# Kernel tuning notes

Measured on AMD Instinct MI355X. Metric: run time of the kernel, lower is better.

## Reference

```python
import jax, jax.numpy as jnp
import numpy as np

N_HEAD = 16
HEAD_SIZE = 64  # n_embd // n_head = 1024 // 16


def setup_inputs() -> dict:
    key = jax.random.key(0)
    k1, k2 = jax.random.split(key)
    B, T, C = 2, 2048, 1024
    x = jax.random.normal(k1, (B, T, C), dtype=jnp.float32)
    w_attn = jax.random.normal(k2, (C, 3 * C), dtype=jnp.float32) * (C ** -0.5)
    b_attn = jnp.zeros((3 * C,), dtype=jnp.float32)
    return {"x": x, "w_attn": w_attn, "b_attn": b_attn}


def reference(x, w_attn, b_attn):
    B, T, C = x.shape
    qkv = x @ w_attn + b_attn  # [B, T, 3C]
    q, k, v = jnp.split(qkv, 3, axis=-1)
    # [B, T, H, D] -> [B, H, T, D]
    def heads(t):
        return t.reshape(B, T, N_HEAD, HEAD_SIZE).transpose(0, 2, 1, 3)
    q, k, v = heads(q), heads(k), heads(v)
    scale = HEAD_SIZE ** -0.5
    wei = jnp.einsum('bhqd,bhkd->bhqk', q, k) * scale  # [B, H, T, T]
    causal = jnp.tril(jnp.ones((T, T), dtype=bool))
    wei = jnp.where(causal, wei, -jnp.inf)
    wei = jax.nn.softmax(wei, axis=-1)
    out = jnp.einsum('bhqk,bhkd->bhqd', wei, v)  # [B, H, T, D]
    out = out.transpose(0, 2, 1, 3).reshape(B, T, C)
    return out
```

## Files before the change

kernel.cpp:

```cpp
#include <hip/hip_runtime.h>
#include <hip/hip_bf16.h>

#define BSZ 2
#define SEQ 2048
#define CDIM 1024
#define NHEAD 16
#define HDIM 64
#define M_GEMM (BSZ * SEQ)
#define N_GEMM (3 * CDIM)
#define K_GEMM CDIM
#define QK_PITCH (2 * CDIM)

typedef __attribute__((ext_vector_type(8))) short short8;
typedef __attribute__((ext_vector_type(4))) short short4v;
typedef __attribute__((ext_vector_type(4))) float f32x4;

__device__ __forceinline__ short bf16_rn(float f) {
    unsigned u = __builtin_bit_cast(unsigned, f);
    u += 0x7FFF + ((u >> 16) & 1);
    return (short)(u >> 16);
}

__device__ __forceinline__ void gl2lds16(const short* g, short* l) {
    __builtin_amdgcn_global_load_lds(
        (const __attribute__((address_space(1))) unsigned int*)g,
        (__attribute__((address_space(3))) unsigned int*)l, 16, 0, 0);
}

#define WAITV2() asm volatile("s_waitcnt vmcnt(2)")
#define WAITV3() asm volatile("s_waitcnt vmcnt(3)")
#define WAITV0() asm volatile("s_waitcnt vmcnt(0)")
#define LGKM0()  asm volatile("s_waitcnt lgkmcnt(0)")
#define SCB()    __builtin_amdgcn_sched_barrier(0)
#define BARRIER() __builtin_amdgcn_s_barrier()

__global__ __launch_bounds__(256) void cvt_fused(const float* __restrict__ X,
                                                 const float* __restrict__ W,
                                                 short* __restrict__ Xb,
                                                 short* __restrict__ WT) {
    const int tid = threadIdx.x;
    if (blockIdx.x < 2048) {
        size_t idx = ((size_t)blockIdx.x * 256 + tid) * 8;
        float4 a = *(const float4*)&X[idx];
        float4 b = *(const float4*)&X[idx + 4];
        short8 o;
        o[0] = bf16_rn(a.x); o[1] = bf16_rn(a.y); o[2] = bf16_rn(a.z); o[3] = bf16_rn(a.w);
        o[4] = bf16_rn(b.x); o[5] = bf16_rn(b.y); o[6] = bf16_rn(b.z); o[7] = bf16_rn(b.w);
        *(short8*)&Xb[idx] = o;
        return;
    }
    __shared__ short T[64][72];
    const int bid = blockIdx.x - 2048;
    const int n0 = (bid % 48) * 64;
    const int k0 = (bid / 48) * 64;
#pragma unroll
    for (int pass = 0; pass < 4; ++pass) {
        int i = pass * 256 + tid;
        int kr = i >> 4;
        int n4 = i & 15;
        float4 v = *(const float4*)&W[(size_t)(k0 + kr) * N_GEMM + n0 + n4 * 4];
        T[n4 * 4 + 0][kr] = bf16_rn(v.x);
        T[n4 * 4 + 1][kr] = bf16_rn(v.y);
        T[n4 * 4 + 2][kr] = bf16_rn(v.z);
        T[n4 * 4 + 3][kr] = bf16_rn(v.w);
    }
    __syncthreads();
#pragma unroll
    for (int pass = 0; pass < 2; ++pass) {
        int o = pass * 256 + tid;
        int nr = o >> 3;
        int c8 = o & 7;
        *(short8*)&WT[(size_t)(n0 + nr) * K_GEMM + k0 + c8 * 8] =
            *(const short8*)&T[nr][c8 * 8];
    }
}

__global__ __launch_bounds__(512, 2) void qkv_gemm_8ph(const short* __restrict__ A,
                                                       const short* __restrict__ Bt,
                                                       const float* __restrict__ bias,
                                                       short* __restrict__ Yqk,
                                                       short* __restrict__ Yv) {
    __shared__ short Asl[32768];
    __shared__ short Bsl[24576];

    const int tid  = threadIdx.x;
    const int w    = tid >> 6;
    const int lane = tid & 63;
    const int l16  = lane & 15;
    const int quad = lane >> 4;
    const int wm   = w >> 2;
    const int wn   = w & 3;
    const int ls   = lane >> 3;
    const int lc   = lane & 7;
    const int fsw  = l16 & 7;

    const int orig = blockIdx.y * 16 + blockIdx.x;
    const int xcd  = orig & 7;
    const int idx  = orig >> 3;
    const int bM   = ((xcd & 1) << 3) + (idx & 7);
    const int bN   = (xcd >> 1) * 4 + (idx >> 3);
    const int m0   = bM << 8;
    const int n0   = bN * 192;

    const short* Ab = A  + (size_t)m0 * K_GEMM;
    const short* Bb = Bt + (size_t)n0 * K_GEMM;

    f32x4 acc[8][3];
#pragma unroll
    for (int i = 0; i < 8; ++i)
#pragma unroll
        for (int j = 0; j < 3; ++j) acc[i][j] = (f32x4){0.f, 0.f, 0.f, 0.f};

    auto stageA = [&](int unit, int tt, int sbuf) {
#pragma unroll
        for (int i = 0; i < 2; ++i) {
            const int u0 = (i * 8 + w) * 8;
            const int tr = (u0 & 63) + ((u0 >> 6) << 7) + unit * 64;
            gl2lds16(Ab + (size_t)(tr + ls) * K_GEMM + tt * 64 + ((lc ^ ls) << 3),
                     &Asl[sbuf * 16384 + tr * 64]);
        }
    };
    auto stageBE = [&](int tt, int sbuf) {
#pragma unroll
        for (int i = 0; i < 2; ++i) {
            const int jb = i * 64 + w * 8;
            const int gr = (jb >> 5) * 48 + (jb & 31);
            gl2lds16(Bb + (size_t)(gr + ls) * K_GEMM + tt * 64 + ((lc ^ ls) << 3),
                     &Bsl[sbuf * 12288 + jb * 64]);
        }
    };
    auto stageBO = [&](int tt, int sbuf) {
        const int t8 = w * 8;
        const int jb = 128 + t8;
        const int gr = (t8 >> 4) * 48 + 32 + (t8 & 15);
        gl2lds16(Bb + (size_t)(gr + ls) * K_GEMM + tt * 64 + ((lc ^ ls) << 3),
                 &Bsl[sbuf * 12288 + jb * 64]);
    };
    auto rdA = [&](int ab, int mi, int ks) -> short8 {
        const int r = wm * 128 + mi * 16 + l16;
        return *(const short8*)&Asl[ab + r * 64 + ((ks * 4 + quad) ^ fsw) * 8];
    };
    auto rdB = [&](int bb, int ni, int ks) -> short8 {
        const int j = (ni < 2) ? (wn * 32 + ni * 16 + l16)
                               : (128 + wn * 16 + l16);
        return *(const short8*)&Bsl[bb + j * 64 + ((ks * 4 + quad) ^ fsw) * 8];
    };

    stageA(0, 0, 0);
    stageBE(0, 0);
    stageA(1, 0, 0);
    stageBO(0, 0);
    WAITV3();
    SCB(); BARRIER(); SCB();

    for (int t = 0; t < 16; ++t) {
        const int buf = t & 1;
        const int sb  = buf ^ 1;
        const int tn  = (t + 1) & 15;
        const int ab  = buf * 16384;
        const int bb  = buf * 12288;

        short8 Af[4][2], Bf[3][2];

#pragma unroll
        for (int mi = 0; mi < 4; ++mi)
#pragma unroll
            for (int ks = 0; ks < 2; ++ks) Af[mi][ks] = rdA(ab, mi, ks);
#pragma unroll
        for (int ni = 0; ni < 2; ++ni)
#pragma unroll
            for (int ks = 0; ks < 2; ++ks) Bf[ni][ks] = rdB(bb, ni, ks);
        stageA(0, tn, sb);
        SCB(); BARRIER(); LGKM0(); SCB();
        __builtin_amdgcn_s_setprio(1);
#pragma unroll
        for (int mi = 0; mi < 4; ++mi)
#pragma unroll
            for (int ni = 0; ni < 2; ++ni)
#pragma unroll
                for (int ks = 0; ks < 2; ++ks)
                    acc[mi][ni] = __builtin_amdgcn_mfma_f32_16x16x32_bf16(
                        Af[mi][ks], Bf[ni][ks], acc[mi][ni], 0, 0, 0);
        __builtin_amdgcn_s_setprio(0);
        WAITV2();
        SCB(); BARRIER(); SCB();

#pragma unroll
        for (int ks = 0; ks < 2; ++ks) Bf[2][ks] = rdB(bb, 2, ks);
        stageBE(tn, sb);
        SCB(); BARRIER(); LGKM0(); SCB();
        __builtin_amdgcn_s_setprio(1);
#pragma unroll
        for (int mi = 0; mi < 4; ++mi)
#pragma unroll
            for (int ks = 0; ks < 2; ++ks)
                acc[mi][2] = __builtin_amdgcn_mfma_f32_16x16x32_bf16(
                    Af[mi][ks], Bf[2][ks], acc[mi][2], 0, 0, 0);
        __builtin_amdgcn_s_setprio(0);
        SCB(); BARRIER(); SCB();

#pragma unroll
        for (int mi = 0; mi < 4; ++mi)
#pragma unroll
            for (int ks = 0; ks < 2; ++ks) Af[mi][ks] = rdA(ab, 4 + mi, ks);
        stageA(1, tn, sb);
        SCB(); BARRIER(); LGKM0(); SCB();
        __builtin_amdgcn_s_setprio(1);
#pragma unroll
        for (int mi = 0; mi < 4; ++mi)
#pragma unroll
            for (int ni = 0; ni < 2; ++ni)
#pragma unroll
                for (int ks = 0; ks < 2; ++ks)
                    acc[4 + mi][ni] = __builtin_amdgcn_mfma_f32_16x16x32_bf16(
                        Af[mi][ks], Bf[ni][ks], acc[4 + mi][ni], 0, 0, 0);
        __builtin_amdgcn_s_setprio(0);
        SCB(); BARRIER(); SCB();

        stageBO(tn, sb);
        SCB(); BARRIER(); SCB();
        __builtin_amdgcn_s_setprio(1);
#pragma unroll
        for (int mi = 0; mi < 4; ++mi)
#pragma unroll
            for (int ks = 0; ks < 2; ++ks)
                acc[4 + mi][2] = __builtin_amdgcn_mfma_f32_16x16x32_bf16(
                    Af[mi][ks], Bf[2][ks], acc[4 + mi][2], 0, 0, 0);
        __builtin_amdgcn_s_setprio(0);
        WAITV3();
        SCB(); BARRIER(); SCB();
    }
    WAITV0();

    const float log2e8 = 0.125f * 1.44269504f;
#pragma unroll
    for (int mi = 0; mi < 8; ++mi) {
#pragma unroll
        for (int ni = 0; ni < 3; ++ni) {
            const int colg = n0 + wn * 48 + ni * 16 + l16;
            const float bb2 = bias[colg];
            if (colg >= 2 * CDIM) {
                const int row0 = m0 + wm * 128 + mi * 16 + quad * 4;
                short4v pk;
#pragma unroll
                for (int r = 0; r < 4; ++r) pk[r] = bf16_rn(acc[mi][ni][r] + bb2);
                *(short4v*)&Yv[(size_t)(colg - 2 * CDIM) * M_GEMM + row0] = pk;
            } else {
                const float qs = (colg < CDIM) ? log2e8 : 1.0f;
#pragma unroll
                for (int r = 0; r < 4; ++r) {
                    const int row = m0 + wm * 128 + mi * 16 + quad * 4 + r;
                    Yqk[(size_t)row * QK_PITCH + colg] =
                        bf16_rn((acc[mi][ni][r] + bb2) * qs);
                }
            }
        }
    }
}

__global__ __launch_bounds__(256) void attn_mfma(const short* __restrict__ qk,
                                                 const short* __restrict__ vT,
                                                 float* __restrict__ out) {
    const int b = blockIdx.z;
    const int h = blockIdx.y;
    const int bx = blockIdx.x;
    const int u = h + 16 * b;
    const int band = u >> 3;
    const int base = (band & 2) ? ((bx + 16) & 31) : bx;
    const int qt = (band & 1) ? (31 - base) : base;
    const int tid = threadIdx.x;
    const int w = tid >> 6;
    const int lane = tid & 63;
    const int quad = lane >> 4;
    const int l16 = lane & 15;
    const int q0 = qt * 64;

    __shared__ short Ks[2][64 * 64];
    __shared__ short Vt[2][64 * 64];

    int koff[2], voff[2], ldso[2];
#pragma unroll
    for (int p = 0; p < 2; ++p) {
        int cid = p * 256 + w * 64 + lane;
        int row = cid >> 3;
        int hK = (row & 3) | (((row >> 3) & 1) << 2);
        int cK = (cid & 7) ^ hK;
        int cV = (cid & 7) ^ (row & 7);
        koff[p] = row * QK_PITCH + cK * 8;
        voff[p] = row * M_GEMM + cV * 8;
        ldso[p] = (p * 256 + w * 64) * 8;
    }

    const short* qrow = qk + (size_t)(b * SEQ + q0 + w * 16 + l16) * QK_PITCH + h * HDIM;
    short8 aq[2];
    aq[0] = *(const short8*)(qrow + quad * 8);
    aq[1] = *(const short8*)(qrow + 32 + quad * 8);

    float l_run = 0.f;
    f32x4 o_acc[4];
#pragma unroll
    for (int dt = 0; dt < 4; ++dt) o_acc[dt] = (f32x4){0.f, 0.f, 0.f, 0.f};

    const int qglob = q0 + w * 16 + l16;
    const short* kb0 = qk + (size_t)(b * SEQ) * QK_PITCH + CDIM + h * HDIM;
    const short* vb0 = vT + (size_t)(h * HDIM) * M_GEMM + b * SEQ;

    const int ksl = l16 & 7;

    const int Fq = ((l16 >> 2) << 3) + (l16 & 3);

#pragma unroll
    for (int p = 0; p < 2; ++p) {
        gl2lds16(kb0 + koff[p], &Ks[0][ldso[p]]);
        gl2lds16(vb0 + voff[p], &Vt[0][ldso[p]]);
    }
    __syncthreads();

    for (int kt = 0; kt <= qt; ++kt) {
        const int cur = kt & 1;

        if (kt < qt) {
            const short* kbase = kb0 + (size_t)(kt + 1) * 64 * QK_PITCH;
            const short* vbase = vb0 + (kt + 1) * 64;
#pragma unroll
            for (int p = 0; p < 2; ++p) {
                gl2lds16(kbase + koff[p], &Ks[cur ^ 1][ldso[p]]);
                gl2lds16(vbase + voff[p], &Vt[cur ^ 1][ldso[p]]);
            }
        }

        const short* KsC = Ks[cur];
        const short* VtC = Vt[cur];

        f32x4 s[4];
#pragma unroll
        for (int nt = 0; nt < 4; ++nt) s[nt] = (f32x4){0.f, 0.f, 0.f, 0.f};
        __builtin_amdgcn_s_setprio(1);
#pragma unroll
        for (int nt = 0; nt < 4; ++nt) {
            const int F  = (nt >> 1) * 32 + (nt & 1) * 4 + Fq;
            const int hF = (F & 3) | (((F >> 3) & 1) << 2);
#pragma unroll
            for (int ks = 0; ks < 2; ++ks) {
                short8 kf = *(const short8*)&KsC[F * 64 + (((ks * 4 + quad) ^ hF) * 8)];
                s[nt] = __builtin_amdgcn_mfma_f32_16x16x32_bf16(kf, aq[ks], s[nt], 0, 0, 0);
            }
        }
        __builtin_amdgcn_s_setprio(0);

        short8 pa0, pa1;
        float lsum = 0.f;
        if (kt < qt) {
#pragma unroll
            for (int nt = 0; nt < 4; ++nt)
#pragma unroll
                for (int r = 0; r < 4; ++r) {
                    float pp = __builtin_amdgcn_exp2f(s[nt][r]);
                    lsum += pp;
                    short pb = bf16_rn(pp);
                    if (nt < 2) pa0[(nt & 1) * 4 + r] = pb;
                    else        pa1[(nt & 1) * 4 + r] = pb;
                }
        } else {
#pragma unroll
            for (int nt = 0; nt < 4; ++nt)
#pragma unroll
                for (int r = 0; r < 4; ++r) {
                    int key = kt * 64 + (nt >> 1) * 32 + quad * 8 + (nt & 1) * 4 + r;
                    float pp = __builtin_amdgcn_exp2f(s[nt][r]);
                    pp = (key > qglob) ? 0.f : pp;
                    lsum += pp;
                    short pb = bf16_rn(pp);
                    if (nt < 2) pa0[(nt & 1) * 4 + r] = pb;
                    else        pa1[(nt & 1) * 4 + r] = pb;
                }
        }
        l_run += lsum;

        __builtin_amdgcn_s_setprio(1);
#pragma unroll
        for (int dt = 0; dt < 4; ++dt)
#pragma unroll
            for (int ks = 0; ks < 2; ++ks) {
                short8 bv = *(const short8*)&VtC[(dt * 16 + l16) * 64 +
                                                 ((ks * 4 + quad) ^ ksl) * 8];
                o_acc[dt] = __builtin_amdgcn_mfma_f32_16x16x32_bf16(
                    ks ? pa1 : pa0, bv, o_acc[dt], 0, 0, 0);
            }
        __builtin_amdgcn_s_setprio(0);

        __syncthreads();
    }

    float l = l_run;
    l += __shfl_xor(l, 16);
    l += __shfl_xor(l, 32);
#pragma unroll
    for (int r = 0; r < 4; ++r) {
        float lq = __shfl(l, quad * 4 + r);
        float inv = 1.f / lq;
        int row = q0 + w * 16 + quad * 4 + r;
        float* optr = out + (size_t)(b * SEQ + row) * CDIM + h * HDIM;
#pragma unroll
        for (int dt = 0; dt < 4; ++dt)
            optr[dt * 16 + l16] = o_acc[dt][r] * inv;
    }
}

extern "C" void kernel_launch(void* const* d_in, const int* in_sizes, int n_in,
                              void* d_out, int out_size, void* d_ws, size_t ws_size,
                              hipStream_t stream) {
    const float* x      = (const float*)d_in[0];
    const float* w_attn = (const float*)d_in[1];
    const float* b_attn = (const float*)d_in[2];
    float* out = (float*)d_out;

    short* qk  = (short*)d_ws;
    short* vT  = (short*)((char*)d_ws + 16777216);
    short* xb  = (short*)((char*)d_ws + 25165824);
    short* wT  = (short*)((char*)d_ws + 33554432);

    cvt_fused<<<2048 + 768, 256, 0, stream>>>(x, w_attn, xb, wT);

    dim3 g1(N_GEMM / 192, M_GEMM / 256);
    qkv_gemm_8ph<<<g1, 512, 0, stream>>>(xb, wT, b_attn, qk, vT);

    dim3 g2(SEQ / 64, NHEAD, BSZ);
    attn_mfma<<<g2, 256, 0, stream>>>(qk, vT, out);
}
```

Measured before the change: 152.5 us.

## Pair complementary causal query tiles in one 512-thread block sharing K/V loads

Each attention block now runs 8 waves covering two query tiles, bx and 31-bx, so causal work per block is balanced. The two tiles share the same double-buffered K/V LDS stages, which halves the global-to-LDS traffic per query tile. The grid is halved to 16x16x2, and the old band-based tile remapping is removed. In exchange, the waves on the short tile sit idle at barriers during the later iterations, and there are fewer, larger blocks to schedule.

```diff
diff --git a/kernel.cpp b/kernel.cpp
--- a/kernel.cpp
+++ b/kernel.cpp
@@ -258,40 +258,38 @@
     }
 }
 
-__global__ __launch_bounds__(256) void attn_mfma(const short* __restrict__ qk,
+__global__ __launch_bounds__(512) void attn_mfma(const short* __restrict__ qk,
                                                  const short* __restrict__ vT,
                                                  float* __restrict__ out) {
     const int b = blockIdx.z;
     const int h = blockIdx.y;
     const int bx = blockIdx.x;
-    const int u = h + 16 * b;
-    const int band = u >> 3;
-    const int base = (band & 2) ? ((bx + 16) & 31) : bx;
-    const int qt = (band & 1) ? (31 - base) : base;
     const int tid = threadIdx.x;
     const int w = tid >> 6;
+    const int ws = w >> 2;
+    const int wq = w & 3;
     const int lane = tid & 63;
     const int quad = lane >> 4;
     const int l16 = lane & 15;
-    const int q0 = qt * 64;
+
+    const int qts   = ws ? (31 - bx) : bx;
+    const int ktmax = 31 - bx;
+    const int q0 = qts * 64;
 
     __shared__ short Ks[2][64 * 64];
     __shared__ short Vt[2][64 * 64];
 
-    int koff[2], voff[2], ldso[2];
-#pragma unroll
-    for (int p = 0; p < 2; ++p) {
-        int cid = p * 256 + w * 64 + lane;
-        int row = cid >> 3;
-        int hK = (row & 3) | (((row >> 3) & 1) << 2);
-        int cK = (cid & 7) ^ hK;
-        int cV = (cid & 7) ^ (row & 7);
-        koff[p] = row * QK_PITCH + cK * 8;
-        voff[p] = row * M_GEMM + cV * 8;
-        ldso[p] = (p * 256 + w * 64) * 8;
-    }
-
-    const short* qrow = qk + (size_t)(b * SEQ + q0 + w * 16 + l16) * QK_PITCH + h * HDIM;
+    int koff, voff, ldso;
+    {
+        const int cid = tid;
+        const int row = cid >> 3;
+        const int hK = (row & 3) | (((row >> 3) & 1) << 2);
+        koff = row * QK_PITCH + (((cid & 7) ^ hK)) * 8;
+        voff = row * M_GEMM + (((cid & 7) ^ (row & 7))) * 8;
+        ldso = (w * 64) * 8;
+    }
+
+    const short* qrow = qk + (size_t)(b * SEQ + q0 + wq * 16 + l16) * QK_PITCH + h * HDIM;
     short8 aq[2];
     aq[0] = *(const short8*)(qrow + quad * 8);
     aq[1] = *(const short8*)(qrow + 32 + quad * 8);
@@ -301,7 +299,7 @@
 #pragma unroll
     for (int dt = 0; dt < 4; ++dt) o_acc[dt] = (f32x4){0.f, 0.f, 0.f, 0.f};
 
-    const int qglob = q0 + w * 16 + l16;
+    const int qglob = q0 + wq * 16 + l16;
     const short* kb0 = qk + (size_t)(b * SEQ) * QK_PITCH + CDIM + h * HDIM;
     const short* vb0 = vT + (size_t)(h * HDIM) * M_GEMM + b * SEQ;
 
@@ -309,85 +307,81 @@
 
     const int Fq = ((l16 >> 2) << 3) + (l16 & 3);
 
-#pragma unroll
-    for (int p = 0; p < 2; ++p) {
-        gl2lds16(kb0 + koff[p], &Ks[0][ldso[p]]);
-        gl2lds16(vb0 + voff[p], &Vt[0][ldso[p]]);
-    }
+    gl2lds16(kb0 + koff, &Ks[0][ldso]);
+    gl2lds16(vb0 + voff, &Vt[0][ldso]);
     __syncthreads();
 
-    for (int kt = 0; kt <= qt; ++kt) {
+    for (int kt = 0; kt <= ktmax; ++kt) {
         const int cur = kt & 1;
 
-        if (kt < qt) {
+        if (kt < ktmax) {
             const short* kbase = kb0 + (size_t)(kt + 1) * 64 * QK_PITCH;
             const short* vbase = vb0 + (kt + 1) * 64;
-#pragma unroll
-            for (int p = 0; p < 2; ++p) {
-                gl2lds16(kbase + koff[p], &Ks[cur ^ 1][ldso[p]]);
-                gl2lds16(vbase + voff[p], &Vt[cur ^ 1][ldso[p]]);
+            gl2lds16(kbase + koff, &Ks[cur ^ 1][ldso]);
+            gl2lds16(vbase + voff, &Vt[cur ^ 1][ldso]);
+        }
+
+        if (kt <= qts) {
+            const short* KsC = Ks[cur];
+            const short* VtC = Vt[cur];
+
+            f32x4 s[4];
+#pragma unroll
+            for (int nt = 0; nt < 4; ++nt) s[nt] = (f32x4){0.f, 0.f, 0.f, 0.f};
+            __builtin_amdgcn_s_setprio(1);
+#pragma unroll
+            for (int nt = 0; nt < 4; ++nt) {
+                const int F  = (nt >> 1) * 32 + (nt & 1) * 4 + Fq;
+                const int hF = (F & 3) | (((F >> 3) & 1) << 2);
+#pragma unroll
+                for (int ks = 0; ks < 2; ++ks) {
+                    short8 kf = *(const short8*)&KsC[F * 64 + (((ks * 4 + quad) ^ hF) * 8)];
+                    s[nt] = __builtin_amdgcn_mfma_f32_16x16x32_bf16(kf, aq[ks], s[nt], 0, 0, 0);
+                }
             }
+            __builtin_amdgcn_s_setprio(0);
+
+            short8 pa0, pa1;
+            float lsum = 0.f;
+            if (kt < qts) {
+#pragma unroll
+                for (int nt = 0; nt < 4; ++nt)
+#pragma unroll
+                    for (int r = 0; r < 4; ++r) {
+                        float pp = __builtin_amdgcn_exp2f(s[nt][r]);
+                        lsum += pp;
+                        short pb = bf16_rn(pp);
+                        if (nt < 2) pa0[(nt & 1) * 4 + r] = pb;
+                        else        pa1[(nt & 1) * 4 + r] = pb;
+                    }
+            } else {
+#pragma unroll
+                for (int nt = 0; nt < 4; ++nt)
+#pragma unroll
+                    for (int r = 0; r < 4; ++r) {
+                        int key = kt * 64 + (nt >> 1) * 32 + quad * 8 + (nt & 1) * 4 + r;
+                        float pp = __builtin_amdgcn_exp2f(s[nt][r]);
+                        pp = (key > qglob) ? 0.f : pp;
+                        lsum += pp;
+                        short pb = bf16_rn(pp);
+                        if (nt < 2) pa0[(nt & 1) * 4 + r] = pb;
+                        else        pa1[(nt & 1) * 4 + r] = pb;
+                    }
+            }
+            l_run += lsum;
+
+            __builtin_amdgcn_s_setprio(1);
+#pragma unroll
+            for (int dt = 0; dt < 4; ++dt)
+#pragma unroll
+                for (int ks = 0; ks < 2; ++ks) {
+                    short8 bv = *(const short8*)&VtC[(dt * 16 + l16) * 64 +
+                                                     ((ks * 4 + quad) ^ ksl) * 8];
+                    o_acc[dt] = __builtin_amdgcn_mfma_f32_16x16x32_bf16(
+                        ks ? pa1 : pa0, bv, o_acc[dt], 0, 0, 0);
+                }
+            __builtin_amdgcn_s_setprio(0);
         }
-
-        const short* KsC = Ks[cur];
-        const short* VtC = Vt[cur];
-
-        f32x4 s[4];
-#pragma unroll
-        for (int nt = 0; nt < 4; ++nt) s[nt] = (f32x4){0.f, 0.f, 0.f, 0.f};
-        __builtin_amdgcn_s_setprio(1);
-#pragma unroll
-        for (int nt = 0; nt < 4; ++nt) {
-            const int F  = (nt >> 1) * 32 + (nt & 1) * 4 + Fq;
-            const int hF = (F & 3) | (((F >> 3) & 1) << 2);
-#pragma unroll
-            for (int ks = 0; ks < 2; ++ks) {
-                short8 kf = *(const short8*)&KsC[F * 64 + (((ks * 4 + quad) ^ hF) * 8)];
-                s[nt] = __builtin_amdgcn_mfma_f32_16x16x32_bf16(kf, aq[ks], s[nt], 0, 0, 0);
-            }
-        }
-        __builtin_amdgcn_s_setprio(0);
-
-        short8 pa0, pa1;
-        float lsum = 0.f;
-        if (kt < qt) {
-#pragma unroll
-            for (int nt = 0; nt < 4; ++nt)
-#pragma unroll
-                for (int r = 0; r < 4; ++r) {
-                    float pp = __builtin_amdgcn_exp2f(s[nt][r]);
-                    lsum += pp;
-                    short pb = bf16_rn(pp);
-                    if (nt < 2) pa0[(nt & 1) * 4 + r] = pb;
-                    else        pa1[(nt & 1) * 4 + r] = pb;
-                }
-        } else {
-#pragma unroll
-            for (int nt = 0; nt < 4; ++nt)
-#pragma unroll
-                for (int r = 0; r < 4; ++r) {
-                    int key = kt * 64 + (nt >> 1) * 32 + quad * 8 + (nt & 1) * 4 + r;
-                    float pp = __builtin_amdgcn_exp2f(s[nt][r]);
-                    pp = (key > qglob) ? 0.f : pp;
-                    lsum += pp;
-                    short pb = bf16_rn(pp);
-                    if (nt < 2) pa0[(nt & 1) * 4 + r] = pb;
-                    else        pa1[(nt & 1) * 4 + r] = pb;
-                }
-        }
-        l_run += lsum;
-
-        __builtin_amdgcn_s_setprio(1);
-#pragma unroll
-        for (int dt = 0; dt < 4; ++dt)
-#pragma unroll
-            for (int ks = 0; ks < 2; ++ks) {
-                short8 bv = *(const short8*)&VtC[(dt * 16 + l16) * 64 +
-                                                 ((ks * 4 + quad) ^ ksl) * 8];
-                o_acc[dt] = __builtin_amdgcn_mfma_f32_16x16x32_bf16(
-                    ks ? pa1 : pa0, bv, o_acc[dt], 0, 0, 0);
-            }
-        __builtin_amdgcn_s_setprio(0);
 
         __syncthreads();
     }
@@ -399,7 +393,7 @@
     for (int r = 0; r < 4; ++r) {
         float lq = __shfl(l, quad * 4 + r);
         float inv = 1.f / lq;
-        int row = q0 + w * 16 + quad * 4 + r;
+        int row = q0 + wq * 16 + quad * 4 + r;
         float* optr = out + (size_t)(b * SEQ + row) * CDIM + h * HDIM;
 #pragma unroll
         for (int dt = 0; dt < 4; ++dt)
@@ -425,6 +419,6 @@
     dim3 g1(N_GEMM / 192, M_GEMM / 256);
     qkv_gemm_8ph<<<g1, 512, 0, stream>>>(xb, wT, b_attn, qk, vT);
 
-    dim3 g2(SEQ / 64, NHEAD, BSZ);
-    attn_mfma<<<g2, 256, 0, stream>>>(qk, vT, out);
-}
+    dim3 g2(SEQ / 128, NHEAD, BSZ);
+    attn_mfma<<<g2, 512, 0, stream>>>(qk, vT, out);
+}
```

New measurement: 150.7 us. Within noise of the previous version (-1.1%).
